# Kernel tuning notes

Measured on AMD Instinct MI355X. Metric: run time of the kernel, lower is better.

## Reference

```python
import jax, jax.numpy as jnp
import numpy as np

B, C, W, H, D = 1, 2, 192, 192, 192


def setup_inputs() -> dict:
    key = jax.random.key(0)
    k1, k2 = jax.random.split(key)
    x = jax.random.normal(k1, (B, C, W, H, D), dtype=jnp.float32)
    # voxel coordinates, slightly outside the FOV to exercise dct2 boundary
    sizes = jnp.array([W, H, D], dtype=jnp.float32)
    u = jax.random.uniform(k2, (B, W, H, D, 3), dtype=jnp.float32)
    grid = u * (sizes + 3.0) - 2.0  # range [-2, n+1]
    return {"x": x, "grid": grid}


def _reflect_dct2(i, n):
    # dct2 / 'reflect' boundary: symmetric about -0.5 and n-0.5, period 2n
    p = 2 * n
    i = jnp.mod(i, p)  # nonnegative result
    return jnp.where(i >= n, p - 1 - i, i)


def reference(x, grid):
    """grid_pull with linear interpolation, dct2 bound, extrapolate=True.
    x: (B, C, W, H, D); grid: (B, W, H, D, 3) in voxel coords -> (B, C, W, H, D)."""
    Bx, Cx, Wx, Hx, Dx = x.shape
    lo = jnp.floor(grid).astype(jnp.int32)          # (B, W, H, D, 3)
    frac = grid - lo.astype(grid.dtype)             # (B, W, H, D, 3)
    flat = x.reshape(Bx, Cx, Wx * Hx * Dx)
    N = grid.shape[1] * grid.shape[2] * grid.shape[3]
    out = jnp.zeros((Bx, Cx, N), dtype=x.dtype)
    for dx in (0, 1):
        wx = frac[..., 0] if dx else 1.0 - frac[..., 0]
        ix = _reflect_dct2(lo[..., 0] + dx, Wx)
        for dy in (0, 1):
            wy = frac[..., 1] if dy else 1.0 - frac[..., 1]
            iy = _reflect_dct2(lo[..., 1] + dy, Hx)
            for dz in (0, 1):
                wz = frac[..., 2] if dz else 1.0 - frac[..., 2]
                iz = _reflect_dct2(lo[..., 2] + dz, Dx)
                idx = ((ix * Hx + iy) * Dx + iz).reshape(Bx, 1, N)
                vals = jnp.take_along_axis(flat, idx, axis=2)  # (B, C, N)
                w = (wx * wy * wz).reshape(Bx, 1, N)
                out = out + vals * w
    return out.reshape(Bx, Cx, *grid.shape[1:4])
```

## Files before the change

### kernel.cpp

```cpp
#include <hip/hip_runtime.h>
#include <hip/hip_fp16.h>


constexpr int DIM = 192;
constexpr int N = DIM * DIM * DIM;
constexpr int C = 2;

constexpr int NBX = DIM / 4;
constexpr int NBY = DIM / 2;
constexpr int NBZ = DIM / 2;
constexpr int NBRICKS = NBX * NBY * NBZ;
constexpr int XSTRIDE = NBY * NBZ * 16;
constexpr int YSTRIDE = NBZ * 16;
constexpr int ZSTRIDE = 16;

typedef float floatx4 __attribute__((ext_vector_type(4)));

__device__ __forceinline__ int reflect_dct2(int i, int n) {
    const int p = 2 * n;
    i = ((i % p) + p) % p;
    return (i >= n) ? (p - 1 - i) : i;
}

__device__ __forceinline__ int xterm(int ix) { return (ix >> 2) * XSTRIDE + ((ix & 3) << 2); }
__device__ __forceinline__ int yterm(int iy) { return (iy >> 1) * YSTRIDE + ((iy & 1) << 1); }
__device__ __forceinline__ int zterm(int iz) { return (iz >> 1) * ZSTRIDE + (iz & 1); }

constexpr int LDS_STRIDE = 200;

__global__ __launch_bounds__(256) void repack_brick_lds_kernel(
        const float* __restrict__ x,
        uint32_t* __restrict__ xb) {
    __shared__ float lds[16 * LDS_STRIDE];

    const int bxy = blockIdx.x;
    const int by  = bxy % NBY;
    const int bx  = bxy / NBY;
    const int tid = threadIdx.x;

#pragma unroll
    for (int k = 0; k < 3; ++k) {
        const int vidx = tid + k * 256;
        const int r    = vidx / 48;
        const int c4   = vidx - r * 48;
        const int c    = r >> 3;
        const int sx   = (r >> 1) & 3;
        const int sy   = r & 1;
        const size_t src = (size_t)c * N
                         + ((size_t)((bx * 4 + sx) * DIM + (by * 2 + sy))) * DIM
                         + (size_t)c4 * 4;
        const floatx4 v = __builtin_nontemporal_load((const floatx4*)(x + src));
        *(floatx4*)(&lds[r * LDS_STRIDE + c4 * 4]) = v;
    }
    __syncthreads();

    for (int slot = tid; slot < NBZ * 4; slot += 256) {
        const int bz = slot >> 2;
        const int q  = slot & 3;
        const int iz = bz * 2;
        const float2 a00 = *(const float2*)&lds[(((0 << 3) | (q << 1) | 0) * LDS_STRIDE) + iz];
        const float2 a01 = *(const float2*)&lds[(((0 << 3) | (q << 1) | 1) * LDS_STRIDE) + iz];
        const float2 a10 = *(const float2*)&lds[(((1 << 3) | (q << 1) | 0) * LDS_STRIDE) + iz];
        const float2 a11 = *(const float2*)&lds[(((1 << 3) | (q << 1) | 1) * LDS_STRIDE) + iz];
        uint4 v;
        v.x = __builtin_bit_cast(uint32_t, __floats2half2_rn(a00.x, a10.x));
        v.y = __builtin_bit_cast(uint32_t, __floats2half2_rn(a00.y, a10.y));
        v.z = __builtin_bit_cast(uint32_t, __floats2half2_rn(a01.x, a11.x));
        v.w = __builtin_bit_cast(uint32_t, __floats2half2_rn(a01.y, a11.y));
        ((uint4*)xb)[(size_t)bxy * (NBZ * 4) + slot] = v;
    }
}

__global__ __launch_bounds__(256) void grid_pull_brick_kernel(
        const uint32_t* __restrict__ xb,
        const float* __restrict__ grid,
        float* __restrict__ out) {
    const int n = blockIdx.x * blockDim.x + threadIdx.x;
    if (n >= N) return;

    const float gx = __builtin_nontemporal_load(&grid[3 * n + 0]);
    const float gy = __builtin_nontemporal_load(&grid[3 * n + 1]);
    const float gz = __builtin_nontemporal_load(&grid[3 * n + 2]);

    const float fx = floorf(gx), fy = floorf(gy), fz = floorf(gz);
    const int lx = (int)fx, ly = (int)fy, lz = (int)fz;
    const float tx = gx - fx, ty = gy - fy, tz = gz - fz;

    const int ix0 = reflect_dct2(lx,     DIM);
    const int ix1 = reflect_dct2(lx + 1, DIM);
    const int iy0 = reflect_dct2(ly,     DIM);
    const int iy1 = reflect_dct2(ly + 1, DIM);
    const int iz0 = reflect_dct2(lz,     DIM);
    const int iz1 = reflect_dct2(lz + 1, DIM);

    const int tx0 = xterm(ix0), tx1 = xterm(ix1);
    const int ty0 = yterm(iy0), ty1 = yterm(iy1);
    const int tz0 = zterm(iz0), tz1 = zterm(iz1);

    const uint32_t u000 = xb[tx0 + ty0 + tz0];
    const uint32_t u001 = xb[tx0 + ty0 + tz1];
    const uint32_t u010 = xb[tx0 + ty1 + tz0];
    const uint32_t u011 = xb[tx0 + ty1 + tz1];
    const uint32_t u100 = xb[tx1 + ty0 + tz0];
    const uint32_t u101 = xb[tx1 + ty0 + tz1];
    const uint32_t u110 = xb[tx1 + ty1 + tz0];
    const uint32_t u111 = xb[tx1 + ty1 + tz1];

    const float wx0 = 1.0f - tx, wx1 = tx;
    const float wy0 = 1.0f - ty, wy1 = ty;
    const float wz0 = 1.0f - tz, wz1 = tz;

    const float w000 = wx0 * wy0 * wz0;
    const float w001 = wx0 * wy0 * wz1;
    const float w010 = wx0 * wy1 * wz0;
    const float w011 = wx0 * wy1 * wz1;
    const float w100 = wx1 * wy0 * wz0;
    const float w101 = wx1 * wy0 * wz1;
    const float w110 = wx1 * wy1 * wz0;
    const float w111 = wx1 * wy1 * wz1;

    const float2 f000 = __half22float2(__builtin_bit_cast(__half2, u000));
    const float2 f001 = __half22float2(__builtin_bit_cast(__half2, u001));
    const float2 f010 = __half22float2(__builtin_bit_cast(__half2, u010));
    const float2 f011 = __half22float2(__builtin_bit_cast(__half2, u011));
    const float2 f100 = __half22float2(__builtin_bit_cast(__half2, u100));
    const float2 f101 = __half22float2(__builtin_bit_cast(__half2, u101));
    const float2 f110 = __half22float2(__builtin_bit_cast(__half2, u110));
    const float2 f111 = __half22float2(__builtin_bit_cast(__half2, u111));

    const float acc0 = f000.x * w000 + f001.x * w001 + f010.x * w010 + f011.x * w011
                     + f100.x * w100 + f101.x * w101 + f110.x * w110 + f111.x * w111;
    const float acc1 = f000.y * w000 + f001.y * w001 + f010.y * w010 + f011.y * w011
                     + f100.y * w100 + f101.y * w101 + f110.y * w110 + f111.y * w111;

    __builtin_nontemporal_store(acc0, &out[n]);
    __builtin_nontemporal_store(acc1, &out[N + n]);
}

__global__ __launch_bounds__(256) void grid_pull_planar_kernel(
        const float* __restrict__ x,
        const float* __restrict__ grid,
        float* __restrict__ out) {
    const int n = blockIdx.x * blockDim.x + threadIdx.x;
    if (n >= N) return;

    const float gx = grid[3 * n + 0];
    const float gy = grid[3 * n + 1];
    const float gz = grid[3 * n + 2];

    const float fx = floorf(gx), fy = floorf(gy), fz = floorf(gz);
    const int lx = (int)fx, ly = (int)fy, lz = (int)fz;
    const float tx = gx - fx, ty = gy - fy, tz = gz - fz;

    const int ix0 = reflect_dct2(lx,     DIM);
    const int ix1 = reflect_dct2(lx + 1, DIM);
    const int iy0 = reflect_dct2(ly,     DIM);
    const int iy1 = reflect_dct2(ly + 1, DIM);
    const int iz0 = reflect_dct2(lz,     DIM);
    const int iz1 = reflect_dct2(lz + 1, DIM);

    const float wx0 = 1.0f - tx, wx1 = tx;
    const float wy0 = 1.0f - ty, wy1 = ty;
    const float wz0 = 1.0f - tz, wz1 = tz;

    const int bx0 = ix0 * (DIM * DIM), bx1 = ix1 * (DIM * DIM);
    const int by0 = iy0 * DIM,         by1 = iy1 * DIM;

    const float w000 = wx0 * wy0 * wz0, w001 = wx0 * wy0 * wz1;
    const float w010 = wx0 * wy1 * wz0, w011 = wx0 * wy1 * wz1;
    const float w100 = wx1 * wy0 * wz0, w101 = wx1 * wy0 * wz1;
    const float w110 = wx1 * wy1 * wz0, w111 = wx1 * wy1 * wz1;

#pragma unroll
    for (int c = 0; c < C; ++c) {
        const float* __restrict__ xc = x + (size_t)c * N;
        float acc = xc[bx0 + by0 + iz0] * w000;
        acc += xc[bx0 + by0 + iz1] * w001;
        acc += xc[bx0 + by1 + iz0] * w010;
        acc += xc[bx0 + by1 + iz1] * w011;
        acc += xc[bx1 + by0 + iz0] * w100;
        acc += xc[bx1 + by0 + iz1] * w101;
        acc += xc[bx1 + by1 + iz0] * w110;
        acc += xc[bx1 + by1 + iz1] * w111;
        out[(size_t)c * N + n] = acc;
    }
}

extern "C" void kernel_launch(void* const* d_in, const int* in_sizes, int n_in,
                              void* d_out, int out_size, void* d_ws, size_t ws_size,
                              hipStream_t stream) {
    const float* x    = (const float*)d_in[0];
    const float* grid = (const float*)d_in[1];
    float* out        = (float*)d_out;

    const int threads = 256;
    const size_t need = (size_t)NBRICKS * 64;

    if (ws_size >= need) {
        uint32_t* xb = (uint32_t*)d_ws;
        repack_brick_lds_kernel<<<NBX * NBY, threads, 0, stream>>>(x, xb);
        const int gblocks = (N + threads - 1) / threads;
        grid_pull_brick_kernel<<<gblocks, threads, 0, stream>>>(xb, grid, out);
    } else {
        const int gblocks = (N + threads - 1) / threads;
        grid_pull_planar_kernel<<<gblocks, threads, 0, stream>>>(x, grid, out);
    }
}
```

Before: 407.6 us.

## Repack input into overlapping halo bricks so each sample needs two vector loads

Adds a repack kernel that, for every (y,z) position, stores the 2x2 y/z neighbourhood of four consecutive x slices (both channels, fp16) as one 16-byte record. The pull kernel then fetches two uint4 records (one per x corner) instead of eight scattered 32-bit gathers, folding the reflected y/z corner weights into Y0/Y1/Z0/Z1. The cost is a workspace four times larger than the non-overlapping brick layout and more repack write traffic. It falls back to the old brick path when the workspace is too small.

```diff
diff --git a/kernel.cpp b/kernel.cpp
--- a/kernel.cpp
+++ b/kernel.cpp
@@ -5,6 +5,128 @@
 constexpr int DIM = 192;
 constexpr int N = DIM * DIM * DIM;
 constexpr int C = 2;
+
+typedef float floatx4 __attribute__((ext_vector_type(4)));
+
+__device__ __forceinline__ int reflect_dct2(int i, int n) {
+    const int p = 2 * n;
+    i = ((i % p) + p) % p;
+    return (i >= n) ? (p - 1 - i) : i;
+}
+
+constexpr size_t HALO_BRICKS = (size_t)(DIM / 4) * DIM * DIM;
+constexpr size_t HALO_BYTES  = HALO_BRICKS * 64;
+
+constexpr int LDS_STRIDE = 200;
+
+__global__ __launch_bounds__(256) void repack_halo_kernel(
+        const float* __restrict__ x,
+        uint32_t* __restrict__ xb) {
+    __shared__ float lds[16 * LDS_STRIDE];
+
+    const int bxy = blockIdx.x;
+    const int y   = bxy % DIM;
+    const int bx  = bxy / DIM;
+    const int tid = threadIdx.x;
+
+#pragma unroll
+    for (int k = 0; k < 3; ++k) {
+        const int vidx = tid + k * 256;
+        const int r    = vidx / 48;
+        const int c4   = vidx - r * 48;
+        const int c    = r >> 3;
+        const int sx   = (r >> 1) & 3;
+        const int ysel = r & 1;
+        const int ysrc = min(y + ysel, DIM - 1);
+        const size_t src = (size_t)c * N
+                         + ((size_t)((bx * 4 + sx) * DIM + ysrc)) * DIM
+                         + (size_t)c4 * 4;
+        const floatx4 v = __builtin_nontemporal_load((const floatx4*)(x + src));
+        *(floatx4*)(&lds[r * LDS_STRIDE + c4 * 4]) = v;
+    }
+    __syncthreads();
+
+#pragma unroll
+    for (int k = 0; k < 3; ++k) {
+        const int t  = tid + k * 256;
+        const int z  = t >> 2;
+        const int q  = t & 3;
+        const int zp = min(z + 1, DIM - 1);
+        const int r00 = q * 2;
+        const int r01 = q * 2 + 1;
+        const int r10 = 8 + q * 2;
+        const int r11 = 8 + q * 2 + 1;
+        uint4 v;
+        v.x = __builtin_bit_cast(uint32_t,
+              __floats2half2_rn(lds[r00 * LDS_STRIDE + z],  lds[r10 * LDS_STRIDE + z]));
+        v.y = __builtin_bit_cast(uint32_t,
+              __floats2half2_rn(lds[r00 * LDS_STRIDE + zp], lds[r10 * LDS_STRIDE + zp]));
+        v.z = __builtin_bit_cast(uint32_t,
+              __floats2half2_rn(lds[r01 * LDS_STRIDE + z],  lds[r11 * LDS_STRIDE + z]));
+        v.w = __builtin_bit_cast(uint32_t,
+              __floats2half2_rn(lds[r01 * LDS_STRIDE + zp], lds[r11 * LDS_STRIDE + zp]));
+        ((uint4*)xb)[(size_t)bxy * (DIM * 4) + t] = v;
+    }
+}
+
+__global__ __launch_bounds__(256) void grid_pull_halo_kernel(
+        const uint32_t* __restrict__ xb,
+        const float* __restrict__ grid,
+        float* __restrict__ out) {
+    const int n = blockIdx.x * blockDim.x + threadIdx.x;
+    if (n >= N) return;
+
+    const float gx = __builtin_nontemporal_load(&grid[3 * n + 0]);
+    const float gy = __builtin_nontemporal_load(&grid[3 * n + 1]);
+    const float gz = __builtin_nontemporal_load(&grid[3 * n + 2]);
+
+    const float fx = floorf(gx), fy = floorf(gy), fz = floorf(gz);
+    const int lx = (int)fx, ly = (int)fy, lz = (int)fz;
+    const float tx = gx - fx, ty = gy - fy, tz = gz - fz;
+
+    const int ix0 = reflect_dct2(lx,     DIM);
+    const int ix1 = reflect_dct2(lx + 1, DIM);
+    const int iy0 = reflect_dct2(ly,     DIM);
+    const int iy1 = reflect_dct2(ly + 1, DIM);
+    const int iz0 = reflect_dct2(lz,     DIM);
+    const int iz1 = reflect_dct2(lz + 1, DIM);
+
+    const int ya = min(iy0, iy1), za = min(iz0, iz1);
+    const int sy0 = iy0 - ya, sy1 = iy1 - ya;
+    const int sz0 = iz0 - za, sz1 = iz1 - za;
+
+    const float wy0 = 1.0f - ty, wy1 = ty;
+    const float wz0 = 1.0f - tz, wz1 = tz;
+
+    const float Y0 = (sy0 ? 0.0f : wy0) + (sy1 ? 0.0f : wy1);
+    const float Y1 = (sy0 ? wy0 : 0.0f) + (sy1 ? wy1 : 0.0f);
+    const float Z0 = (sz0 ? 0.0f : wz0) + (sz1 ? 0.0f : wz1);
+    const float Z1 = (sz0 ? wz0 : 0.0f) + (sz1 ? wz1 : 0.0f);
+
+    const size_t d0 = ((size_t)(((ix0 >> 2) * DIM + ya) * DIM + za) << 4) + ((ix0 & 3) << 2);
+    const size_t d1 = ((size_t)(((ix1 >> 2) * DIM + ya) * DIM + za) << 4) + ((ix1 & 3) << 2);
+    const uint4 v0 = *(const uint4*)(xb + d0);
+    const uint4 v1 = *(const uint4*)(xb + d1);
+
+    const float2 a00 = __half22float2(__builtin_bit_cast(__half2, v0.x));
+    const float2 a01 = __half22float2(__builtin_bit_cast(__half2, v0.y));
+    const float2 a10 = __half22float2(__builtin_bit_cast(__half2, v0.z));
+    const float2 a11 = __half22float2(__builtin_bit_cast(__half2, v0.w));
+    const float2 b00 = __half22float2(__builtin_bit_cast(__half2, v1.x));
+    const float2 b01 = __half22float2(__builtin_bit_cast(__half2, v1.y));
+    const float2 b10 = __half22float2(__builtin_bit_cast(__half2, v1.z));
+    const float2 b11 = __half22float2(__builtin_bit_cast(__half2, v1.w));
+
+    const float wx0 = 1.0f - tx, wx1 = tx;
+
+    const float acc0 = wx0 * (Y0 * (Z0 * a00.x + Z1 * a01.x) + Y1 * (Z0 * a10.x + Z1 * a11.x))
+                     + wx1 * (Y0 * (Z0 * b00.x + Z1 * b01.x) + Y1 * (Z0 * b10.x + Z1 * b11.x));
+    const float acc1 = wx0 * (Y0 * (Z0 * a00.y + Z1 * a01.y) + Y1 * (Z0 * a10.y + Z1 * a11.y))
+                     + wx1 * (Y0 * (Z0 * b00.y + Z1 * b01.y) + Y1 * (Z0 * b10.y + Z1 * b11.y));
+
+    __builtin_nontemporal_store(acc0, &out[n]);
+    __builtin_nontemporal_store(acc1, &out[N + n]);
+}
 
 constexpr int NBX = DIM / 4;
 constexpr int NBY = DIM / 2;
@@ -14,19 +136,9 @@
 constexpr int YSTRIDE = NBZ * 16;
 constexpr int ZSTRIDE = 16;
 
-typedef float floatx4 __attribute__((ext_vector_type(4)));
-
-__device__ __forceinline__ int reflect_dct2(int i, int n) {
-    const int p = 2 * n;
-    i = ((i % p) + p) % p;
-    return (i >= n) ? (p - 1 - i) : i;
-}
-
 __device__ __forceinline__ int xterm(int ix) { return (ix >> 2) * XSTRIDE + ((ix & 3) << 2); }
 __device__ __forceinline__ int yterm(int iy) { return (iy >> 1) * YSTRIDE + ((iy & 1) << 1); }
 __device__ __forceinline__ int zterm(int iz) { return (iz >> 1) * ZSTRIDE + (iz & 1); }
-
-constexpr int LDS_STRIDE = 200;
 
 __global__ __launch_bounds__(256) void repack_brick_lds_kernel(
         const float* __restrict__ x,
@@ -110,14 +222,10 @@
     const float wy0 = 1.0f - ty, wy1 = ty;
     const float wz0 = 1.0f - tz, wz1 = tz;
 
-    const float w000 = wx0 * wy0 * wz0;
-    const float w001 = wx0 * wy0 * wz1;
-    const float w010 = wx0 * wy1 * wz0;
-    const float w011 = wx0 * wy1 * wz1;
-    const float w100 = wx1 * wy0 * wz0;
-    const float w101 = wx1 * wy0 * wz1;
-    const float w110 = wx1 * wy1 * wz0;
-    const float w111 = wx1 * wy1 * wz1;
+    const float w000 = wx0 * wy0 * wz0, w001 = wx0 * wy0 * wz1;
+    const float w010 = wx0 * wy1 * wz0, w011 = wx0 * wy1 * wz1;
+    const float w100 = wx1 * wy0 * wz0, w101 = wx1 * wy0 * wz1;
+    const float w110 = wx1 * wy1 * wz0, w111 = wx1 * wy1 * wz1;
 
     const float2 f000 = __half22float2(__builtin_bit_cast(__half2, u000));
     const float2 f001 = __half22float2(__builtin_bit_cast(__half2, u001));
@@ -194,15 +302,18 @@
     float* out        = (float*)d_out;
 
     const int threads = 256;
-    const size_t need = (size_t)NBRICKS * 64;
-
-    if (ws_size >= need) {
+    const int gblocks = (N + threads - 1) / threads;
+    const size_t need_brick = (size_t)NBRICKS * 64;
+
+    if (ws_size >= HALO_BYTES) {
+        uint32_t* xb = (uint32_t*)d_ws;
+        repack_halo_kernel<<<(DIM / 4) * DIM, threads, 0, stream>>>(x, xb);
+        grid_pull_halo_kernel<<<gblocks, threads, 0, stream>>>(xb, grid, out);
+    } else if (ws_size >= need_brick) {
         uint32_t* xb = (uint32_t*)d_ws;
         repack_brick_lds_kernel<<<NBX * NBY, threads, 0, stream>>>(x, xb);
-        const int gblocks = (N + threads - 1) / threads;
         grid_pull_brick_kernel<<<gblocks, threads, 0, stream>>>(xb, grid, out);
     } else {
-        const int gblocks = (N + threads - 1) / threads;
         grid_pull_planar_kernel<<<gblocks, threads, 0, stream>>>(x, grid, out);
     }
 }
```

New measurement: 338.2 us. 1.21x faster.
